# Performance work log

Measured on AMD Instinct MI355X. Metric: run time of the kernel, lower is better.

## Reference

```python
import jax, jax.numpy as jnp
import numpy as np

# Dims: B latent vectors processed through T sequential LALR-state calls.
B, T = 4096, 128      # batch of latent vecs, timesteps
NL = 256              # n_latent (scaled up from default 100)
NS = 64               # number of LALR states with learned layers
NO = 32               # output tokens per state (Linear(n_latent, n_out))
V = 64                # len(terminals): size of scattered output vector


def setup_inputs() -> dict:
    key = jax.random.key(0)
    ks = jax.random.split(key, 7)
    return {
        "latent0": jax.random.normal(ks[0], (B, NL), jnp.float32),
        "W1": jax.random.normal(ks[1], (NS, NL, NL), jnp.float32) / np.sqrt(NL).astype(np.float32),
        "b1": jax.random.normal(ks[2], (NS, NL), jnp.float32) * 0.01,
        "W2": jax.random.normal(ks[3], (NS, NO, NL), jnp.float32) / np.sqrt(NL).astype(np.float32),
        "b2": jax.random.normal(ks[4], (NS, NO), jnp.float32) * 0.01,
        "state_seq": jax.random.randint(ks[5], (T,), 0, NS, jnp.int32),
        "out_idx": jax.random.randint(ks[6], (NS, NO), 0, V, jnp.int32),
    }


def reference(latent0, W1, b1, W2, b2, state_seq, out_idx):
    """Per-timestep LALR state call:
       newlatent = tanh(Linear(x));
       probs     = softmax(Linear(newlatent));
       output    = IndicesExpansion: scatter probs into zeros(V) at out_idx[state].
    State weights are gathered by state id; batch is processed jointly."""
    def step(x, s):
        w1, bb1 = W1[s], b1[s]            # [NL,NL], [NL]
        w2, bb2 = W2[s], b2[s]            # [NO,NL], [NO]
        idx = out_idx[s]                  # [NO]
        x_new = jnp.tanh(x @ w1.T + bb1)                       # [B, NL]
        probs = jax.nn.softmax(x_new @ w2.T + bb2, axis=-1)    # [B, NO]
        # IndicesExpansionLayer: zero vector of size V, set vals at indices
        y = jnp.zeros((x.shape[0], V), x.dtype).at[:, idx].set(probs)
        return x_new, y

    final_latent, ys = jax.lax.scan(step, latent0, state_seq)  # ys: [T, B, V]
    return jnp.transpose(ys, (1, 0, 2))  # [B, T, V]
```

## Files before the change

kernel.cpp:

```cpp
#include <hip/hip_runtime.h>

#define B_  4096
#define T_  128
#define NL  256
#define NS  64
#define NO  32
#define V_  64
#define RB  16
#define NBLK (B_ / RB)

typedef __bf16 bf16;
typedef bf16  bf16x8 __attribute__((ext_vector_type(8)));
typedef bf16  bf16x4 __attribute__((ext_vector_type(4)));
typedef float f32x4  __attribute__((ext_vector_type(4)));

#define MF(a, b, c) __builtin_amdgcn_mfma_f32_16x16x32_bf16(a, b, c, 0, 0, 0)

#define LGKM_BARRIER() asm volatile("s_waitcnt lgkmcnt(0)\n\ts_barrier" ::: "memory")

template <int TSHIFT>
__global__ void split_w_frag(const float* __restrict__ src,
                             bf16* __restrict__ hi, bf16* __restrict__ lo,
                             int total4) {
    int t4 = blockIdx.x * blockDim.x + threadIdx.x;
    if (t4 >= total4) return;
    const int jb   = (t4 & 1) * 4;
    const int L    = (t4 >> 1) & 63;
    const int ks   = (t4 >> 7) & 7;
    const int rest = t4 >> 10;
    const int t    = rest & ((1 << TSHIFT) - 1);
    const int s    = rest >> TSHIFT;
    const int row  = ((s << TSHIFT) + t) * 16 + (L & 15);
    const int k    = ks * 32 + (L >> 4) * 8 + jb;
    const float4 v = *(const float4*)(src + (size_t)row * NL + k);
    float vv[4] = {v.x, v.y, v.z, v.w};
    bf16x4 h, l;
#pragma unroll
    for (int e = 0; e < 4; e++) {
        bf16 hh = (bf16)vv[e];
        h[e] = hh;
        l[e] = (bf16)(vv[e] - (float)hh);
    }
    *(bf16x4*)(hi + (size_t)t4 * 4) = h;
    *(bf16x4*)(lo + (size_t)t4 * 4) = l;
}

__global__ void inv_kernel(const int* __restrict__ out_idx, int* __restrict__ inv) {
    int t = blockIdx.x * blockDim.x + threadIdx.x;
    if (t >= NS * V_) return;
    int s = t >> 6, v = t & 63;
    int jf = -1;
#pragma unroll
    for (int j = 0; j < NO; j++)
        if (out_idx[(s << 5) | j] == v) jf = j;
    inv[t] = jf;
}

__device__ __forceinline__ float fast_tanh(float z) {
    float e = __expf(2.0f * z);
    return 1.0f - 2.0f / (e + 1.0f);
}

__device__ __forceinline__ int xaddr(int t, int q, int n) {
    return ((t >> 1) * 512) + (((t & 1) * 2 + (q >> 1)) * 128) + n * 8 + (q & 1) * 4;
}

__launch_bounds__(1024, 4)
__global__ void lalr_main(const float* __restrict__ latent0,
                          const float* __restrict__ b1,
                          const float* __restrict__ b2,
                          const int*   __restrict__ state_seq,
                          const int*   __restrict__ inv,
                          const bf16*  __restrict__ W1h, const bf16* __restrict__ W1l,
                          const bf16*  __restrict__ W2h, const bf16* __restrict__ W2l,
                          float* __restrict__ out) {
    __shared__ bf16  xh[2][4096];
    __shared__ bf16  xl[2][4096];
    __shared__ float Sp[2][8][16][36];

    const int tid  = threadIdx.x;
    const int wave = tid >> 6;
    const int lane = tid & 63;
    const int n    = lane & 15;
    const int q    = lane >> 4;
    const int r0   = blockIdx.x * RB;
    const int t2   = wave & 1;
    const int ks2  = wave >> 1;

    {
        float4 v = *(const float4*)(latent0 + (size_t)(r0 + n) * NL + wave * 16 + q * 4);
        float vv[4] = {v.x, v.y, v.z, v.w};
        bf16x4 hv, lv;
#pragma unroll
        for (int e = 0; e < 4; e++) {
            bf16 hh = (bf16)vv[e];
            hv[e] = hh;
            lv[e] = (bf16)(vv[e] - (float)hh);
        }
        const int a = xaddr(wave, q, n);
        *(bf16x4*)(&xh[0][a]) = hv;
        *(bf16x4*)(&xl[0][a]) = lv;
    }

    int s0 = state_seq[0], s1 = -1, s2 = -1;

    bf16x8 pwh[8], pwl[8];
    {
        const bf16* w1hb = W1h + ((size_t)(s0 * 16 + wave) * 8) * 512;
        const bf16* w1lb = W1l + ((size_t)(s0 * 16 + wave) * 8) * 512;
#pragma unroll
        for (int p = 0; p < 8; p++) {
            pwh[p] = *(const bf16x8*)(w1hb + p * 512 + lane * 8);
            pwl[p] = *(const bf16x8*)(w1lb + p * 512 + lane * 8);
        }
    }
    bf16x8 w2h2, w2l2;

    LGKM_BARRIER();

    for (int i = 0; i <= T_ + 1; i++) {
        const int ib  = i & 1;
        const int cur = ib;

        f32x4 acc1;
        if (s0 >= 0) {
            acc1 = (f32x4){0.f, 0.f, 0.f, 0.f};
#pragma unroll
            for (int ks = 0; ks < 8; ks++) {
                bf16x8 xa = *(const bf16x8*)(&xh[cur][ks * 512 + lane * 8]);
                bf16x8 xb = *(const bf16x8*)(&xl[cur][ks * 512 + lane * 8]);
                acc1 = MF(pwh[ks], xa, acc1);
                acc1 = MF(pwl[ks], xa, acc1);
                acc1 = MF(pwh[ks], xb, acc1);
            }
        }

        if (s1 >= 0) {
            bf16x8 xa = *(const bf16x8*)(&xh[cur][ks2 * 512 + lane * 8]);
            bf16x8 xb = *(const bf16x8*)(&xl[cur][ks2 * 512 + lane * 8]);
            f32x4 a2 = (f32x4){0.f, 0.f, 0.f, 0.f};
            a2 = MF(w2h2, xa, a2);
            a2 = MF(w2l2, xa, a2);
            a2 = MF(w2h2, xb, a2);
            if (ks2 == 0) {
                float4 bb = *(const float4*)(b2 + s1 * NO + t2 * 16 + q * 4);
                a2[0] += bb.x; a2[1] += bb.y; a2[2] += bb.z; a2[3] += bb.w;
            }
            *(f32x4*)(&Sp[ib][ks2][n][t2 * 16 + q * 4]) = a2;
        }

        const int ns0 = (i + 1 < T_) ? state_seq[i + 1] : -1;
        if (ns0 >= 0) {
            const bf16* w1hb = W1h + ((size_t)(ns0 * 16 + wave) * 8) * 512;
            const bf16* w1lb = W1l + ((size_t)(ns0 * 16 + wave) * 8) * 512;
#pragma unroll
            for (int p = 0; p < 8; p++) {
                pwh[p] = *(const bf16x8*)(w1hb + p * 512 + lane * 8);
                pwl[p] = *(const bf16x8*)(w1lb + p * 512 + lane * 8);
            }
        }
        if (s0 >= 0) {
            const bf16* w2hb = W2h + ((size_t)((s0 * 2 + t2) * 8 + ks2)) * 512;
            const bf16* w2lb = W2l + ((size_t)((s0 * 2 + t2) * 8 + ks2)) * 512;
            w2h2 = *(const bf16x8*)(w2hb + lane * 8);
            w2l2 = *(const bf16x8*)(w2lb + lane * 8);
        }

        if (s2 >= 0 && tid < 256) {
            const int r  = tid >> 4;
            const int j0 = tid & 15;
            const int pb = (i - 1) & 1;
            float v0 = 0.f, v1 = 0.f;
#pragma unroll
            for (int w = 0; w < 8; w++) {
                v0 += Sp[pb][w][r][j0];
                v1 += Sp[pb][w][r][j0 + 16];
            }
            float m = fmaxf(v0, v1);
#pragma unroll
            for (int d = 1; d < 16; d <<= 1) m = fmaxf(m, __shfl_xor(m, d));
            float e0 = __expf(v0 - m), e1 = __expf(v1 - m);
            float su = e0 + e1;
#pragma unroll
            for (int d = 1; d < 16; d <<= 1) su += __shfl_xor(su, d);
            float is = 1.0f / su;
            float p0 = e0 * is, p1 = e1 * is;
            const int gb = lane & 48;
            int4 iv4 = *(const int4*)(inv + s2 * V_ + j0 * 4);
            int ivv[4] = {iv4.x, iv4.y, iv4.z, iv4.w};
            float o[4];
#pragma unroll
            for (int e = 0; e < 4; e++) {
                float ga = __shfl(p0, gb + (ivv[e] & 15));
                float gc = __shfl(p1, gb + (ivv[e] & 15));
                o[e] = (ivv[e] < 0) ? 0.f : ((ivv[e] < 16) ? ga : gc);
            }
            *(float4*)(out + ((size_t)(r0 + r) * T_ + (i - 2)) * V_ + j0 * 4) = *(float4*)o;
        }

        if (s0 >= 0) {
            float4 bb = *(const float4*)(b1 + s0 * NL + wave * 16 + q * 4);
            float bv[4] = {bb.x, bb.y, bb.z, bb.w};
            bf16x4 hv, lv;
#pragma unroll
            for (int e = 0; e < 4; e++) {
                float h = fast_tanh(acc1[e] + bv[e]);
                bf16 hh = (bf16)h;
                hv[e] = hh;
                lv[e] = (bf16)(h - (float)hh);
            }
            const int a = xaddr(wave, q, n);
            *(bf16x4*)(&xh[cur ^ 1][a]) = hv;
            *(bf16x4*)(&xl[cur ^ 1][a]) = lv;
        }

        s2 = s1; s1 = s0; s0 = ns0;
        LGKM_BARRIER();
    }
}

extern "C" void kernel_launch(void* const* d_in, const int* in_sizes, int n_in,
                              void* d_out, int out_size, void* d_ws, size_t ws_size,
                              hipStream_t stream) {
    const float* latent0   = (const float*)d_in[0];
    const float* W1        = (const float*)d_in[1];
    const float* b1        = (const float*)d_in[2];
    const float* W2        = (const float*)d_in[3];
    const float* b2        = (const float*)d_in[4];
    const int*   state_seq = (const int*)d_in[5];
    const int*   out_idx   = (const int*)d_in[6];
    float* out = (float*)d_out;

    bf16* W1h = (bf16*)d_ws;
    bf16* W1l = W1h + (size_t)NS * NL * NL;
    bf16* W2h = W1l + (size_t)NS * NL * NL;
    bf16* W2l = W2h + (size_t)NS * NO * NL;
    int*  inv = (int*)(W2l + (size_t)NS * NO * NL);

    const int n4_w1 = NS * NL * NL / 4;
    const int n4_w2 = NS * NO * NL / 4;
    split_w_frag<4><<<n4_w1 / 256, 256, 0, stream>>>(W1, W1h, W1l, n4_w1);
    split_w_frag<1><<<n4_w2 / 256, 256, 0, stream>>>(W2, W2h, W2l, n4_w2);
    inv_kernel<<<(NS * V_ + 255) / 256, 256, 0, stream>>>(out_idx, inv);

    lalr_main<<<NBLK, 1024, 0, stream>>>(latent0, b1, b2, state_seq, inv,
                                         W1h, W1l, W2h, W2l, out);
}
```

Before: 629.9 us.

## Pipeline W1 fragment prefetch with inline-asm loads and stage bias tables in LDS

Replaces compiler-scheduled weight loads with inline-asm global_load_dwordx4 plus explicit vmcnt waits, so each k-slice's next-state W1 fragment is issued right after its MFMAs consume the current registers, overlapping the next step's weight fetch with compute. It also copies b1, b2, the inverse index table and the state sequence into shared memory once at kernel start, so per-step bias and index lookups read LDS instead of global memory. This adds a large LDS footprint (b1 alone is 64 KB), which may limit occupancy or exceed the LDS limit. The hand-counted vmcnt values are fragile if the compiler emits other vector memory ops.

```diff
diff --git a/kernel.cpp b/kernel.cpp
--- a/kernel.cpp
+++ b/kernel.cpp
@@ -17,6 +17,10 @@
 #define MF(a, b, c) __builtin_amdgcn_mfma_f32_16x16x32_bf16(a, b, c, 0, 0, 0)
 
 #define LGKM_BARRIER() asm volatile("s_waitcnt lgkmcnt(0)\n\ts_barrier" ::: "memory")
+
+#define GLOAD(dst, ptr, off) \
+    asm volatile("global_load_dwordx4 %0, %1, off offset:" #off \
+                 : "=v"(dst) : "v"(ptr))
 
 template <int TSHIFT>
 __global__ void split_w_frag(const float* __restrict__ src,
@@ -77,6 +81,10 @@
     __shared__ bf16  xh[2][4096];
     __shared__ bf16  xl[2][4096];
     __shared__ float Sp[2][8][16][36];
+    __shared__ float b1s[NS * NL];
+    __shared__ float b2s[NS * NO];
+    __shared__ int   invs[NS * V_];
+    __shared__ int   sseq[T_];
 
     const int tid  = threadIdx.x;
     const int wave = tid >> 6;
@@ -87,6 +95,12 @@
     const int t2   = wave & 1;
     const int ks2  = wave >> 1;
 
+    for (int k = tid; k < NS * NL / 4; k += 1024)
+        ((float4*)b1s)[k] = ((const float4*)b1)[k];
+    if (tid < NS * NO / 4) ((float4*)b2s)[tid] = ((const float4*)b2)[tid];
+    if (tid < NS * V_ / 4) ((int4*)invs)[tid] = ((const int4*)inv)[tid];
+    if (tid < T_) sseq[tid] = state_seq[tid];
+
     {
         float4 v = *(const float4*)(latent0 + (size_t)(r0 + n) * NL + wave * 16 + q * 4);
         float vv[4] = {v.x, v.y, v.z, v.w};
@@ -95,7 +109,7 @@
         for (int e = 0; e < 4; e++) {
             bf16 hh = (bf16)vv[e];
             hv[e] = hh;
-            lv[e] = (bf16)(vv[e] - (float)hh);
+            lv[e] = (bf16)(vv[e] - (float)hv[e]);
         }
         const int a = xaddr(wave, q, n);
         *(bf16x4*)(&xh[0][a]) = hv;
@@ -104,66 +118,92 @@
 
     int s0 = state_seq[0], s1 = -1, s2 = -1;
 
-    bf16x8 pwh[8], pwl[8];
+    bf16x8 pwh0, pwh1, pwh2, pwh3, pwh4, pwh5, pwh6, pwh7;
+    bf16x8 pwl0, pwl1, pwl2, pwl3, pwl4, pwl5, pwl6, pwl7;
+    bf16x8 w2h2, w2l2;
+
+    const size_t wfrag = (size_t)wave * 8 * 512 + lane * 8;
+
     {
-        const bf16* w1hb = W1h + ((size_t)(s0 * 16 + wave) * 8) * 512;
-        const bf16* w1lb = W1l + ((size_t)(s0 * 16 + wave) * 8) * 512;
-#pragma unroll
-        for (int p = 0; p < 8; p++) {
-            pwh[p] = *(const bf16x8*)(w1hb + p * 512 + lane * 8);
-            pwl[p] = *(const bf16x8*)(w1lb + p * 512 + lane * 8);
-        }
-    }
-    bf16x8 w2h2, w2l2;
+        const bf16* h0 = W1h + (size_t)s0 * 16 * 8 * 512 + wfrag;
+        const bf16* l0 = W1l + (size_t)s0 * 16 * 8 * 512 + wfrag;
+        const bf16* h4 = h0 + 4 * 512;
+        const bf16* l4 = l0 + 4 * 512;
+        GLOAD(pwh0, h0, 0);    GLOAD(pwl0, l0, 0);
+        GLOAD(pwh1, h0, 1024); GLOAD(pwl1, l0, 1024);
+        GLOAD(pwh2, h0, 2048); GLOAD(pwl2, l0, 2048);
+        GLOAD(pwh3, h0, 3072); GLOAD(pwl3, l0, 3072);
+        GLOAD(pwh4, h4, 0);    GLOAD(pwl4, l4, 0);
+        GLOAD(pwh5, h4, 1024); GLOAD(pwl5, l4, 1024);
+        GLOAD(pwh6, h4, 2048); GLOAD(pwl6, l4, 2048);
+        GLOAD(pwh7, h4, 3072); GLOAD(pwl7, l4, 3072);
+        const bf16* c2h = W2h + (size_t)((s0 * 2 + t2) * 8 + ks2) * 512 + lane * 8;
+        const bf16* c2l = W2l + (size_t)((s0 * 2 + t2) * 8 + ks2) * 512 + lane * 8;
+        GLOAD(w2h2, c2h, 0);   GLOAD(w2l2, c2l, 0);
+    }
 
     LGKM_BARRIER();
+
+#define G1S(ks, ph, pl, off) {                                              \
+        bf16x8 xa = *(const bf16x8*)(&xh[cur][ks * 512 + lane * 8]);        \
+        bf16x8 xb = *(const bf16x8*)(&xl[cur][ks * 512 + lane * 8]);        \
+        asm volatile("s_waitcnt vmcnt(16)" ::: "memory");                   \
+        __builtin_amdgcn_sched_barrier(0);                                  \
+        acc1 = MF(pwh##ks, xa, acc1);                                       \
+        acc1 = MF(pwl##ks, xa, acc1);                                       \
+        acc1 = MF(pwh##ks, xb, acc1);                                       \
+        GLOAD(pwh##ks, ph, off);                                            \
+        GLOAD(pwl##ks, pl, off);                                            \
+    }
 
     for (int i = 0; i <= T_ + 1; i++) {
         const int ib  = i & 1;
         const int cur = ib;
 
+        const int ns0 = (i + 1 < T_) ? sseq[i + 1] : -1;
+        const int ls  = (ns0 >= 0) ? ns0 : 0;
+        const bf16* nh0 = W1h + (size_t)ls * 16 * 8 * 512 + wfrag;
+        const bf16* nl0 = W1l + (size_t)ls * 16 * 8 * 512 + wfrag;
+        const bf16* nh4 = nh0 + 4 * 512;
+        const bf16* nl4 = nl0 + 4 * 512;
+
         f32x4 acc1;
         if (s0 >= 0) {
             acc1 = (f32x4){0.f, 0.f, 0.f, 0.f};
-#pragma unroll
-            for (int ks = 0; ks < 8; ks++) {
-                bf16x8 xa = *(const bf16x8*)(&xh[cur][ks * 512 + lane * 8]);
-                bf16x8 xb = *(const bf16x8*)(&xl[cur][ks * 512 + lane * 8]);
-                acc1 = MF(pwh[ks], xa, acc1);
-                acc1 = MF(pwl[ks], xa, acc1);
-                acc1 = MF(pwh[ks], xb, acc1);
-            }
+            G1S(0, nh0, nl0, 0)
+            G1S(1, nh0, nl0, 1024)
+            G1S(2, nh0, nl0, 2048)
+            G1S(3, nh0, nl0, 3072)
+            G1S(4, nh4, nl4, 0)
+            G1S(5, nh4, nl4, 1024)
+            G1S(6, nh4, nl4, 2048)
+            G1S(7, nh4, nl4, 3072)
         }
 
         if (s1 >= 0) {
             bf16x8 xa = *(const bf16x8*)(&xh[cur][ks2 * 512 + lane * 8]);
             bf16x8 xb = *(const bf16x8*)(&xl[cur][ks2 * 512 + lane * 8]);
+            if (s0 >= 0) {
+                asm volatile("s_waitcnt vmcnt(16)" ::: "memory");
+            } else {
+                asm volatile("s_waitcnt vmcnt(0)" ::: "memory");
+            }
+            __builtin_amdgcn_sched_barrier(0);
             f32x4 a2 = (f32x4){0.f, 0.f, 0.f, 0.f};
             a2 = MF(w2h2, xa, a2);
             a2 = MF(w2l2, xa, a2);
             a2 = MF(w2h2, xb, a2);
             if (ks2 == 0) {
-                float4 bb = *(const float4*)(b2 + s1 * NO + t2 * 16 + q * 4);
+                float4 bb = *(const float4*)(&b2s[s1 * NO + t2 * 16 + q * 4]);
                 a2[0] += bb.x; a2[1] += bb.y; a2[2] += bb.z; a2[3] += bb.w;
             }
             *(f32x4*)(&Sp[ib][ks2][n][t2 * 16 + q * 4]) = a2;
         }
-
-        const int ns0 = (i + 1 < T_) ? state_seq[i + 1] : -1;
-        if (ns0 >= 0) {
-            const bf16* w1hb = W1h + ((size_t)(ns0 * 16 + wave) * 8) * 512;
-            const bf16* w1lb = W1l + ((size_t)(ns0 * 16 + wave) * 8) * 512;
-#pragma unroll
-            for (int p = 0; p < 8; p++) {
-                pwh[p] = *(const bf16x8*)(w1hb + p * 512 + lane * 8);
-                pwl[p] = *(const bf16x8*)(w1lb + p * 512 + lane * 8);
-            }
-        }
         if (s0 >= 0) {
-            const bf16* w2hb = W2h + ((size_t)((s0 * 2 + t2) * 8 + ks2)) * 512;
-            const bf16* w2lb = W2l + ((size_t)((s0 * 2 + t2) * 8 + ks2)) * 512;
-            w2h2 = *(const bf16x8*)(w2hb + lane * 8);
-            w2l2 = *(const bf16x8*)(w2lb + lane * 8);
+            const bf16* n2h = W2h + (size_t)((s0 * 2 + t2) * 8 + ks2) * 512 + lane * 8;
+            const bf16* n2l = W2l + (size_t)((s0 * 2 + t2) * 8 + ks2) * 512 + lane * 8;
+            GLOAD(w2h2, n2h, 0);
+            GLOAD(w2l2, n2l, 0);
         }
 
         if (s2 >= 0 && tid < 256) {
@@ -186,7 +226,7 @@
             float is = 1.0f / su;
             float p0 = e0 * is, p1 = e1 * is;
             const int gb = lane & 48;
-            int4 iv4 = *(const int4*)(inv + s2 * V_ + j0 * 4);
+            int4 iv4 = *(const int4*)(&invs[s2 * V_ + j0 * 4]);
             int ivv[4] = {iv4.x, iv4.y, iv4.z, iv4.w};
             float o[4];
 #pragma unroll
@@ -199,7 +239,7 @@
         }
 
         if (s0 >= 0) {
-            float4 bb = *(const float4*)(b1 + s0 * NL + wave * 16 + q * 4);
+            float4 bb = *(const float4*)(&b1s[s0 * NL + wave * 16 + q * 4]);
             float bv[4] = {bb.x, bb.y, bb.z, bb.w};
             bf16x4 hv, lv;
 #pragma unroll
@@ -217,6 +257,7 @@
         s2 = s1; s1 = s0; s0 = ns0;
         LGKM_BARRIER();
     }
+#undef G1S
 }
 
 extern "C" void kernel_launch(void* const* d_in, const int* in_sizes, int n_in,
```

New measurement: 550.9 us. -12.5%, faster.
